# Performance work log

Measured on AMD Instinct MI355X. Metric: run time of the kernel, lower is better.

The kernel has to match this reference:

```python
import jax, jax.numpy as jnp
import numpy as np
import math

H = 8                 # num_heads
MAX_REL = 32          # max_relative_distance
VOCAB_REL = 2 * MAX_REL + 1


def setup_inputs() -> dict:
    key = jax.random.key(0)
    ks = jax.random.split(key, 8)
    B, S, D = 4, 2048, 256
    hd = D // H
    sd = 1.0 / math.sqrt(D)
    inp = {
        "query": jax.random.normal(ks[0], (B, S, D), jnp.float32),
        "mask": jnp.ones((B, 1, 1, S), jnp.float32),
        "Wq": jax.random.normal(ks[1], (D, D), jnp.float32) * sd,
        "bq": jnp.zeros((D,), jnp.float32),
        "Wk": jax.random.normal(ks[2], (D, D), jnp.float32) * sd,
        "bk": jnp.zeros((D,), jnp.float32),
        "Wv": jax.random.normal(ks[3], (D, D), jnp.float32) * sd,
        "bv": jnp.zeros((D,), jnp.float32),
        "Wo": jax.random.normal(ks[4], (D, D), jnp.float32) * sd,
        "bo": jnp.zeros((D,), jnp.float32),
        "rel_table": jax.random.normal(ks[5], (VOCAB_REL, hd), jnp.float32) * 0.1,
    }
    return inp


def _split_heads(x, B, S, hd):
    # [B,S,D] -> [B,H,S,hd]
    return x.reshape(B, S, H, hd).transpose(0, 2, 1, 3)


def _relative_row_sums(S, rel_table):
    # Original: emb = table[relpos]  (S,S,hd); scores += einsum('bhid,jkd->bhijk', Q, emb).sum(-1)
    # == einsum('bhid,jd->bhij', Q, R) with R[j,d] = sum_k emb[j,k,d].
    # Compute R without materializing the (S,S,hd) tensor: count how often each
    # relative-position bucket appears in each row, then counts @ table.
    pos = jnp.arange(S)
    relpos = jnp.clip(pos[:, None] - pos[None, :], -MAX_REL, MAX_REL) + MAX_REL  # [S,S] ints
    rows = jnp.broadcast_to(pos[:, None], (S, S))
    counts = jnp.zeros((S, VOCAB_REL), rel_table.dtype).at[
        rows.reshape(-1), relpos.reshape(-1)
    ].add(1.0)
    return counts @ rel_table  # [S, hd]


def reference(query, mask, Wq, bq, Wk, bk, Wv, bv, Wo, bo, rel_table):
    B, S, D = query.shape
    hd = D // H
    scale = 1.0 / math.sqrt(hd)

    Q = _split_heads(query @ Wq + bq, B, S, hd)
    K = _split_heads(query @ Wk + bk, B, S, hd)   # key defaults to query
    V = _split_heads(query @ Wv + bv, B, S, hd)   # value defaults to key

    scores = jnp.einsum("bhid,bhjd->bhij", Q, K) * scale
    R = _relative_row_sums(S, rel_table)          # [S, hd]
    scores = scores + jnp.einsum("bhid,jd->bhij", Q, R)

    scores = scores + (1.0 - mask) * -1e9         # mask broadcast [B,1,1,S]
    attn = jax.nn.softmax(scores, axis=-1)        # dropout is identity (training=False)

    out = jnp.einsum("bhij,bhjd->bhid", attn, V)
    out = out.transpose(0, 2, 1, 3).reshape(B, S, D)
    return out @ Wo + bo
```

## Files before the change

kernel.cpp:

```cpp
#include <hip/hip_runtime.h>
#include <hip/hip_bf16.h>
#include <math.h>

#define NH 8
#define HD 32
#define SEQ 2048
#define DM 256
#define SCALE 0.17677669529663687f
#define INV_SCALE 5.656854249492381f
#define LOG2E 1.4426950408889634f
#define QSC (SCALE * LOG2E)
#define MNEG (-1e9f * LOG2E)

typedef float f32x4 __attribute__((ext_vector_type(4)));
typedef __bf16 bf16x8 __attribute__((ext_vector_type(8)));

#define GLOAD(g, l) __builtin_amdgcn_global_load_lds( \
    (const __attribute__((address_space(1))) void*)(g), \
    (__attribute__((address_space(3))) void*)(l), 16, 0, 0)

__global__ void k_prep(const float* __restrict__ query, const float* __restrict__ mask,
                       const float* __restrict__ Wq, const float* __restrict__ Wk,
                       const float* __restrict__ Wv, const float* __restrict__ Wo,
                       const float* __restrict__ bq, const float* __restrict__ tbl,
                       __bf16* __restrict__ Xb, __bf16* __restrict__ Wt,
                       __bf16* __restrict__ WoT, float* __restrict__ MT,
                       __bf16* __restrict__ SUFn, __bf16* __restrict__ PREn,
                       float* __restrict__ WV2T, float* __restrict__ cb,
                       int* __restrict__ MFLAG) {
  const int blk = blockIdx.x, tid = threadIdx.x;
  __shared__ float ts[64][65];
  __shared__ int okl;
  if (blk < 1024) {
    size_t i = (size_t)blk * 2048 + (size_t)tid * 8;
    float4 a = *(const float4*)(query + i);
    float4 b4 = *(const float4*)(query + i + 4);
    union { __bf16 h[8]; bf16x8 v; } o;
    o.h[0] = (__bf16)a.x;  o.h[1] = (__bf16)a.y;
    o.h[2] = (__bf16)a.z;  o.h[3] = (__bf16)a.w;
    o.h[4] = (__bf16)b4.x; o.h[5] = (__bf16)b4.y;
    o.h[6] = (__bf16)b4.z; o.h[7] = (__bf16)b4.w;
    *(bf16x8*)(Xb + i) = o.v;
  } else if (blk < 1088) {
    const int idx = blk - 1024;
    const float* W;
    __bf16* dst;
    int tile;
    if (idx < 48) {
      int which = idx >> 4;
      W = which == 0 ? Wq : (which == 1 ? Wk : Wv);
      dst = Wt + which * 65536;
      tile = idx & 15;
    } else {
      W = Wo; dst = WoT; tile = idx - 48;
    }
    const int tr = (tile >> 2) * 64, tc = (tile & 3) * 64;
#pragma unroll
    for (int p = 0; p < 4; ++p) {
      int row = p * 16 + (tid >> 4);
      int col = (tid & 15) * 4;
      float4 v = *(const float4*)(W + (size_t)(tr + row) * 256 + tc + col);
      ts[row][col] = v.x; ts[row][col + 1] = v.y;
      ts[row][col + 2] = v.z; ts[row][col + 3] = v.w;
    }
    __syncthreads();
#pragma unroll
    for (int p = 0; p < 2; ++p) {
      int n = p * 32 + (tid >> 3);
      int kb = (tid & 7) * 8;
      union { __bf16 h[8]; bf16x8 v; } o;
#pragma unroll
      for (int e = 0; e < 8; ++e) o.h[e] = (__bf16)ts[kb + e][n];
      *(bf16x8*)(dst + (size_t)(tc + n) * 256 + tr + kb) = o.v;
    }
  } else if (blk == 1088) {
    if (tid == 0) okl = 1;
    __syncthreads();
    bool ok = true;
    for (int i = tid; i < 4 * SEQ; i += 256) {
      float mv = mask[i];
      MT[i] = (1.0f - mv) * MNEG;
      ok &= (mv == 1.0f);
    }
    if (!ok) atomicAnd(&okl, 0);
    __syncthreads();
    if (tid == 0) MFLAG[0] = okl;
  } else if (blk == 1089) {
    for (int idx = tid; idx < 1024; idx += 256) {
      int j = idx >> 5, d = idx & 31;
      float s = 0.f;
      for (int u = j + 33; u <= 63; ++u) s += tbl[u * 32 + d];
      SUFn[idx] = (__bf16)(-s * INV_SCALE);
    }
    for (int idx = tid; idx < 1024; idx += 256) {
      int jj = idx >> 5, d = idx & 31;
      float s = 0.f;
      for (int u = 1; u <= jj; ++u) s += tbl[u * 32 + d];
      PREn[idx] = (__bf16)(-s * INV_SCALE);
    }
  } else if (blk < 1106) {
    int tg = (blk - 1090) * 256 + tid;
    int hv = tg >> 8, k = tg & 255;
    const float* T = tbl + ((hv & 1) ? 0 : 64 * 32);
    const float* w = Wq + (size_t)k * 256 + (hv >> 1) * 32;
    float acc = 0.f;
#pragma unroll
    for (int d = 0; d < 32; ++d) acc = fmaf(w[d], T[d], acc);
    WV2T[hv * 256 + k] = acc * LOG2E;
  } else {
    if (tid < 16) {
      const float* T = tbl + ((tid & 1) ? 0 : 64 * 32);
      float a = 0.f;
#pragma unroll
      for (int d = 0; d < 32; ++d) a = fmaf(bq[(tid >> 1) * 32 + d], T[d], a);
      cb[tid] = a * LOG2E;
    }
  }
}

__launch_bounds__(256)
__global__ void k_rel(const float* __restrict__ X, const float* __restrict__ WV2T,
                      const float* __restrict__ cb, float* __restrict__ REL) {
  __shared__ float Xs[32][260];
  __shared__ float Ws[16][260];
  const int tid = threadIdx.x;
  const size_t base = (size_t)blockIdx.x * 32 * 256;
#pragma unroll
  for (int p = 0; p < 8; ++p) {
    int idx = p * 1024 + tid * 4;
    float4 v = *(const float4*)(X + base + idx);
    *(float4*)&Xs[idx >> 8][idx & 255] = v;
  }
#pragma unroll
  for (int p = 0; p < 4; ++p) {
    int idx = p * 1024 + tid * 4;
    float4 v = *(const float4*)(WV2T + idx);
    *(float4*)&Ws[idx >> 8][idx & 255] = v;
  }
  __syncthreads();
  const int hv = tid & 15, rl = tid >> 4;
  float a0 = cb[hv], a1 = a0;
  const float* xs0 = &Xs[rl][0];
  const float* xs1 = &Xs[rl + 16][0];
  const float* wsp = &Ws[hv][0];
#pragma unroll 8
  for (int k = 0; k < 256; ++k) {
    float w = wsp[k];
    a0 = fmaf(xs0[k], w, a0);
    a1 = fmaf(xs1[k], w, a1);
  }
  const int row0 = blockIdx.x * 32 + rl;
  const int h = hv >> 1, v = hv & 1;
  const int b0i = row0 >> 11, s0 = row0 & 2047;
  REL[((size_t)(b0i * NH + h) * SEQ + s0) * 2 + v] = a0;
  const int r1 = row0 + 16;
  const int b1i = r1 >> 11, s1 = r1 & 2047;
  REL[((size_t)(b1i * NH + h) * SEQ + s1) * 2 + v] = a1;
}

template <int MODE>
__launch_bounds__(256)
__global__ void k_gemm(const __bf16* __restrict__ A, const __bf16* __restrict__ Bt,
                       const float* __restrict__ b0, const float* __restrict__ b1,
                       const float* __restrict__ b2,
                       __bf16* __restrict__ Qb, __bf16* __restrict__ Kb,
                       __bf16* __restrict__ VTout, float* __restrict__ Y) {
  constexpr int BN = (MODE == 0) ? 128 : 64;
  constexpr int NFJ = BN / 32;
  __shared__ __align__(16) __bf16 As[128 * 64];
  __shared__ __align__(16) __bf16 Bs[BN * 64];
  const int tid = threadIdx.x, lane = tid & 63, wid = tid >> 6;
  const int l16 = lane & 15, lhi = lane >> 4;
  const int wr = wid >> 1, wc = wid & 1;
  const int m0 = blockIdx.x * 128, n0 = blockIdx.y * BN;

  f32x4 acc[4][NFJ];
#pragma unroll
  for (int i = 0; i < 4; ++i)
#pragma unroll
    for (int j = 0; j < NFJ; ++j) acc[i][j] = (f32x4){0.f, 0.f, 0.f, 0.f};

  for (int k0 = 0; k0 < 256; k0 += 64) {
    __syncthreads();
#pragma unroll
    for (int cc = 0; cc < 4; ++cc) {
      int cl = tid + cc * 256;
      int row = cl >> 3, kc = cl & 7;
      int k = k0 + ((kc ^ (row & 7)) * 8);
      const __bf16* src;
      if constexpr (MODE == 0) {
        src = A + (size_t)(m0 + row) * 256 + k;
      } else {
        int r = m0 + row, bb = r >> 11, s = r & 2047, h = k >> 5, dh = k & 31;
        src = A + ((size_t)(bb * NH + h) * SEQ + s) * HD + dh;
      }
      GLOAD(src, (__bf16*)As + (size_t)cl * 8);
    }
#pragma unroll
    for (int cc = 0; cc < NFJ; ++cc) {
      int cl = tid + cc * 256;
      int row = cl >> 3, kc = cl & 7;
      int k = k0 + ((kc ^ (row & 7)) * 8);
      GLOAD(Bt + (size_t)(n0 + row) * 256 + k, (__bf16*)Bs + (size_t)cl * 8);
    }
    __syncthreads();
#pragma unroll
    for (int kk = 0; kk < 64; kk += 32) {
      bf16x8 af[4], bfr[NFJ];
#pragma unroll
      for (int fi = 0; fi < 4; ++fi) {
        int row = wr * 64 + fi * 16 + l16;
        af[fi] = *(const bf16x8*)(As + row * 64 + ((((kk >> 3) + lhi) ^ (row & 7)) * 8));
      }
#pragma unroll
      for (int fj = 0; fj < NFJ; ++fj) {
        int row = wc * (BN / 2) + fj * 16 + l16;
        bfr[fj] = *(const bf16x8*)(Bs + row * 64 + ((((kk >> 3) + lhi) ^ (row & 7)) * 8));
      }
#pragma unroll
      for (int fi = 0; fi < 4; ++fi)
#pragma unroll
        for (int fj = 0; fj < NFJ; ++fj)
          acc[fi][fj] = __builtin_amdgcn_mfma_f32_16x16x32_bf16(af[fi], bfr[fj], acc[fi][fj], 0, 0, 0);
    }
  }
#pragma unroll
  for (int fi = 0; fi < 4; ++fi) {
#pragma unroll
    for (int fj = 0; fj < NFJ; ++fj) {
      int mrow = m0 + wr * 64 + fi * 16 + lhi * 4;
      int ncol = n0 + wc * (BN / 2) + fj * 16 + l16;
      if constexpr (MODE == 0) {
        int which = ncol >> 8, nw = ncol & 255, h = nw >> 5, dh = nw & 31;
        int bb = mrow >> 11, s0 = mrow & 2047;
        if (which == 2) {
          union { __bf16 h4[4]; uint2 u; } o;
#pragma unroll
          for (int r = 0; r < 4; ++r) o.h4[r] = (__bf16)(acc[fi][fj][r] + b2[nw]);
          *(uint2*)(VTout + ((size_t)(bb * NH + h) * HD + dh) * SEQ + s0) = o.u;
        } else {
          const float* bias = which == 0 ? b0 : b1;
#pragma unroll
          for (int r = 0; r < 4; ++r) {
            float v = acc[fi][fj][r] + bias[nw];
            size_t oi = ((size_t)(bb * NH + h) * SEQ + (s0 + r)) * HD + dh;
            if (which == 0) Qb[oi] = (__bf16)(v * QSC);
            else Kb[oi] = (__bf16)v;
          }
        }
      } else {
#pragma unroll
        for (int r = 0; r < 4; ++r)
          Y[(size_t)(mrow + r) * 256 + ncol] = acc[fi][fj][r] + b0[ncol];
      }
    }
  }
}

__launch_bounds__(512, 4)
__global__ void k_flash(const __bf16* __restrict__ Qb, const __bf16* __restrict__ Kb,
                        const __bf16* __restrict__ VT, const float* __restrict__ REL,
                        const __bf16* __restrict__ SUFn, const __bf16* __restrict__ PREn,
                        const float* __restrict__ MT, const int* __restrict__ MFLAG,
                        __bf16* __restrict__ Ob) {
  const int bh = blockIdx.y, qt = blockIdx.x, b = bh >> 3;
  const int tid = threadIdx.x, wid = tid >> 6, lane = tid & 63;
  const int l16 = lane & 15, lhi = lane >> 4;

  __shared__ __align__(16) __bf16 kbuf[2][128 * 32];
  __shared__ __align__(16) __bf16 vbuf[2][32 * 128];
  __shared__ __align__(16) __bf16 plds[8][16 * 128];

  const int qrow = qt * 128 + wid * 16 + l16;
  const size_t rg = (size_t)bh * SEQ + qrow;
  const bf16x8 qfrag = *(const bf16x8*)(Qb + rg * HD + lhi * 8);
  const float2 uw = *(const float2*)(REL + rg * 2);
  const float uu = uw.x, ww = uw.y, duw = uu - ww;
  const float duw16 = 16.f * duw;
  const f32x4 duwr = {0.f, duw, 2.f * duw, 3.f * duw};
  const int flag = MFLAG[0];

  const int kj = tid >> 2, kc = tid & 3;
  const __bf16* ksrc = Kb + (size_t)bh * SEQ * HD + (size_t)kj * HD + ((kc ^ ((kj >> 1) & 3)) * 8);
  const int vd = tid >> 4, vc = tid & 15;
  const __bf16* vsrc = VT + ((size_t)bh * HD + vd) * SEQ + ((vc ^ (vd & 7)) * 8);

  f32x4 of0 = {0.f, 0.f, 0.f, 0.f}, of1 = {0.f, 0.f, 0.f, 0.f}, of2 = {0.f, 0.f, 0.f, 0.f};
  const f32x4 zero4 = {0.f, 0.f, 0.f, 0.f}; (void)zero4;
  bf16x8 ones;
#pragma unroll
  for (int e = 0; e < 8; ++e) ones[e] = (__bf16)1.0f;
  float m = -3.0e38f;
  __bf16* pl = &plds[wid][0];
  const float* mtp = MT + b * SEQ + lhi * 4;

  GLOAD(ksrc, &kbuf[0][(size_t)tid * 8]);
  GLOAD(vsrc, &vbuf[0][(size_t)tid * 8]);
  __syncthreads();

  for (int t = 0, cur = 0; t < 16; ++t, cur ^= 1) {
    const int jb = t * 128;
    if (t < 15) {
      GLOAD(ksrc + (size_t)(jb + 128) * HD, &kbuf[cur ^ 1][(size_t)tid * 8]);
      GLOAD(vsrc + (jb + 128), &vbuf[cur ^ 1][(size_t)tid * 8]);
    }
    const __bf16* kb = kbuf[cur];
    const __bf16* vb = vbuf[cur];

    f32x4 lin = duwr + (float)(jb + lhi * 4) * duw;
    f32x4 sf[8];
    __builtin_amdgcn_s_setprio(1);
#pragma unroll
    for (int jt = 0; jt < 8; ++jt) {
      const int row = jt * 16 + l16;
      bf16x8 kf = *(const bf16x8*)(kb + row * 32 + ((lhi ^ ((row >> 1) & 3)) * 8));
      sf[jt] = __builtin_amdgcn_mfma_f32_16x16x32_bf16(kf, qfrag, lin, 0, 0, 0);
      lin += duw16;
    }
    __builtin_amdgcn_s_setprio(0);

    if (t == 0) {
      const bf16x8 s0 = *(const bf16x8*)(SUFn + l16 * HD + lhi * 8);
      const bf16x8 s1 = *(const bf16x8*)(SUFn + (16 + l16) * HD + lhi * 8);
      sf[0] = __builtin_amdgcn_mfma_f32_16x16x32_bf16(s0, qfrag, sf[0], 0, 0, 0);
      sf[1] = __builtin_amdgcn_mfma_f32_16x16x32_bf16(s1, qfrag, sf[1], 0, 0, 0);
#pragma unroll
      for (int jt = 0; jt < 2; ++jt)
#pragma unroll
        for (int r = 0; r < 4; ++r)
          sf[jt][r] += fmaxf(31.f - (float)(jt * 16 + lhi * 4 + r), 0.f) * uu;
    }
    if (t == 15) {
      const bf16x8 p0 = *(const bf16x8*)(PREn + l16 * HD + lhi * 8);
      const bf16x8 p1 = *(const bf16x8*)(PREn + (16 + l16) * HD + lhi * 8);
      sf[6] = __builtin_amdgcn_mfma_f32_16x16x32_bf16(p0, qfrag, sf[6], 0, 0, 0);
      sf[7] = __builtin_amdgcn_mfma_f32_16x16x32_bf16(p1, qfrag, sf[7], 0, 0, 0);
#pragma unroll
      for (int jt = 6; jt < 8; ++jt)
#pragma unroll
        for (int r = 0; r < 4; ++r)
          sf[jt][r] += fmaxf((float)(1920 + jt * 16 + lhi * 4 + r) - 2016.f, 0.f) * ww;
    }
    if (!flag) {
#pragma unroll
      for (int jt = 0; jt < 8; ++jt)
        sf[jt] += *(const f32x4*)(mtp + jb + jt * 16);
    }

    float tmax = -3.0e38f;
#pragma unroll
    for (int jt = 0; jt < 8; ++jt)
      tmax = fmaxf(tmax, fmaxf(fmaxf(sf[jt].x, sf[jt].y), fmaxf(sf[jt].z, sf[jt].w)));
    tmax = fmaxf(tmax, __shfl_xor(tmax, 16));
    tmax = fmaxf(tmax, __shfl_xor(tmax, 32));
    const float mn = fmaxf(m, tmax);
    const float c = __builtin_amdgcn_exp2f(m - mn);
    m = mn;
    of0 *= c; of1 *= c; of2 *= c;

#pragma unroll
    for (int jt = 0; jt < 8; ++jt) {
      union { __bf16 h4[4]; uint2 u; } pk;
#pragma unroll
      for (int r = 0; r < 4; ++r)
        pk.h4[r] = (__bf16)__builtin_amdgcn_exp2f(sf[jt][r] - m);
      const int blk16 = ((jt * 2 + (lhi >> 1)) ^ (l16 & 7));
      *(uint2*)(pl + l16 * 128 + blk16 * 8 + (lhi & 1) * 4) = pk.u;
    }

    __builtin_amdgcn_s_setprio(1);
#pragma unroll
    for (int kt = 0; kt < 4; ++kt) {
      const int pblk = (kt * 4 + lhi) ^ (l16 & 7);
      bf16x8 pf = *(const bf16x8*)(pl + l16 * 128 + pblk * 8);
      bf16x8 v0 = *(const bf16x8*)(vb + l16 * 128 + (((kt * 4 + lhi) ^ (l16 & 7)) * 8));
      bf16x8 v1 = *(const bf16x8*)(vb + (16 + l16) * 128 + (((kt * 4 + lhi) ^ (l16 & 7)) * 8));
      of0 = __builtin_amdgcn_mfma_f32_16x16x32_bf16(v0, pf, of0, 0, 0, 0);
      of1 = __builtin_amdgcn_mfma_f32_16x16x32_bf16(v1, pf, of1, 0, 0, 0);
      of2 = __builtin_amdgcn_mfma_f32_16x16x32_bf16(ones, pf, of2, 0, 0, 0);
    }
    __builtin_amdgcn_s_setprio(0);
    __syncthreads();
  }

  const float inv = 1.0f / of2[0];
  union { __bf16 h4[4]; uint2 u; } o0, o1;
#pragma unroll
  for (int r = 0; r < 4; ++r) {
    o0.h4[r] = (__bf16)(of0[r] * inv);
    o1.h4[r] = (__bf16)(of1[r] * inv);
  }
  *(uint2*)(Ob + rg * HD + lhi * 4) = o0.u;
  *(uint2*)(Ob + rg * HD + 16 + lhi * 4) = o1.u;
}

extern "C" void kernel_launch(void* const* d_in, const int* in_sizes, int n_in,
                              void* d_out, int out_size, void* d_ws, size_t ws_size,
                              hipStream_t stream) {
  (void)in_sizes; (void)n_in; (void)out_size; (void)ws_size;
  const float* query = (const float*)d_in[0];
  const float* mask  = (const float*)d_in[1];
  const float* Wq = (const float*)d_in[2];
  const float* bq = (const float*)d_in[3];
  const float* Wk = (const float*)d_in[4];
  const float* bk = (const float*)d_in[5];
  const float* Wv = (const float*)d_in[6];
  const float* bv = (const float*)d_in[7];
  const float* Wo = (const float*)d_in[8];
  const float* bo = (const float*)d_in[9];
  const float* tbl = (const float*)d_in[10];
  float* out = (float*)d_out;
  char* ws = (char*)d_ws;

  const size_t MB = 1024ull * 1024;
  __bf16* Xb    = (__bf16*)(ws);
  __bf16* Wt    = (__bf16*)(ws + 4 * MB);
  __bf16* WoT   = (__bf16*)(ws + 4 * MB + 393216);
  __bf16* SUFn  = (__bf16*)(ws + 4 * MB + 524288);
  __bf16* PREn  = (__bf16*)(ws + 4 * MB + 526336);
  float*  WV2T  = (float*) (ws + 4 * MB + 528384);
  float*  cbv   = (float*) (ws + 4 * MB + 544768);
  float*  MT    = (float*) (ws + 4 * MB + 544832);
  int*    MFLAG = (int*)   (ws + 4 * MB + 577600);
  float*  REL   = (float*) (ws + 5 * MB);
  __bf16* Qb    = (__bf16*)(ws + 6 * MB);
  __bf16* Kb    = (__bf16*)(ws + 10 * MB);
  __bf16* VT    = (__bf16*)(ws + 14 * MB);
  __bf16* Ob    = (__bf16*)(ws + 18 * MB);

  k_prep<<<1107, 256, 0, stream>>>(query, mask, Wq, Wk, Wv, Wo, bq, tbl,
                                   Xb, Wt, WoT, MT, SUFn, PREn, WV2T, cbv, MFLAG);
  k_rel<<<256, 256, 0, stream>>>(query, WV2T, cbv, REL);
  k_gemm<0><<<dim3(64, 6), 256, 0, stream>>>(Xb, Wt, bq, bk, bv, Qb, Kb, VT, nullptr);
  k_flash<<<dim3(16, 32), 512, 0, stream>>>(Qb, Kb, VT, REL, SUFn, PREn, MT, MFLAG, Ob);
  k_gemm<1><<<dim3(64, 4), 256, 0, stream>>>(Ob, WoT, bo, nullptr, nullptr,
                                             nullptr, nullptr, nullptr, out);
}
```

Baseline: 89.65 us.

## Split P staging into two halves, hoist linear bias, remap flash block order

The flash kernel now precomputes the per-column linear relative-bias term once, as constant accumulator seeds. The per-tile offset jb*duw is folded into the running max instead of being added to every score. The softmax-exp, P store and PV MFMA stage is split into two half-tile phases, which halves the P LDS buffer and lets the exp work of one half interleave with the MFMAs of the other. The grid is flattened to 1D with a block-to-(batch,head) mapping that spreads heads across XCDs for cache locality. The max is computed on unshifted scores, which slightly changes numerical rounding, and it adds 32 registers for c0.

```diff
diff --git a/kernel.cpp b/kernel.cpp
--- a/kernel.cpp
+++ b/kernel.cpp
@@ -263,30 +263,39 @@
                         const __bf16* __restrict__ SUFn, const __bf16* __restrict__ PREn,
                         const float* __restrict__ MT, const int* __restrict__ MFLAG,
                         __bf16* __restrict__ Ob) {
-  const int bh = blockIdx.y, qt = blockIdx.x, b = bh >> 3;
+  const int bid = blockIdx.x;
+  const int bh = (bid & 7) * 4 + ((bid >> 3) & 3);
+  const int qt = bid >> 5;
+  const int b = bh >> 3;
   const int tid = threadIdx.x, wid = tid >> 6, lane = tid & 63;
   const int l16 = lane & 15, lhi = lane >> 4;
 
   __shared__ __align__(16) __bf16 kbuf[2][128 * 32];
   __shared__ __align__(16) __bf16 vbuf[2][32 * 128];
-  __shared__ __align__(16) __bf16 plds[8][16 * 128];
+  __shared__ __align__(16) __bf16 plds[8][16 * 64];
 
   const int qrow = qt * 128 + wid * 16 + l16;
   const size_t rg = (size_t)bh * SEQ + qrow;
   const bf16x8 qfrag = *(const bf16x8*)(Qb + rg * HD + lhi * 8);
   const float2 uw = *(const float2*)(REL + rg * 2);
   const float uu = uw.x, ww = uw.y, duw = uu - ww;
-  const float duw16 = 16.f * duw;
-  const f32x4 duwr = {0.f, duw, 2.f * duw, 3.f * duw};
   const int flag = MFLAG[0];
 
+  f32x4 c0[8];
+  {
+    const f32x4 cr = {(float)(lhi * 4) * duw, (float)(lhi * 4 + 1) * duw,
+                      (float)(lhi * 4 + 2) * duw, (float)(lhi * 4 + 3) * duw};
+#pragma unroll
+    for (int jt = 0; jt < 8; ++jt)
+      c0[jt] = cr + (float)(jt * 16) * duw;
+  }
+
   const int kj = tid >> 2, kc = tid & 3;
-  const __bf16* ksrc = Kb + (size_t)bh * SEQ * HD + (size_t)kj * HD + ((kc ^ ((kj >> 1) & 3)) * 8);
+  const __bf16* ksrc = Kb + ((size_t)bh * SEQ + kj) * HD + ((kc ^ ((kj >> 1) & 3)) * 8);
   const int vd = tid >> 4, vc = tid & 15;
   const __bf16* vsrc = VT + ((size_t)bh * HD + vd) * SEQ + ((vc ^ (vd & 7)) * 8);
 
   f32x4 of0 = {0.f, 0.f, 0.f, 0.f}, of1 = {0.f, 0.f, 0.f, 0.f}, of2 = {0.f, 0.f, 0.f, 0.f};
-  const f32x4 zero4 = {0.f, 0.f, 0.f, 0.f}; (void)zero4;
   bf16x8 ones;
 #pragma unroll
   for (int e = 0; e < 8; ++e) ones[e] = (__bf16)1.0f;
@@ -307,15 +316,13 @@
     const __bf16* kb = kbuf[cur];
     const __bf16* vb = vbuf[cur];
 
-    f32x4 lin = duwr + (float)(jb + lhi * 4) * duw;
     f32x4 sf[8];
     __builtin_amdgcn_s_setprio(1);
 #pragma unroll
     for (int jt = 0; jt < 8; ++jt) {
       const int row = jt * 16 + l16;
       bf16x8 kf = *(const bf16x8*)(kb + row * 32 + ((lhi ^ ((row >> 1) & 3)) * 8));
-      sf[jt] = __builtin_amdgcn_mfma_f32_16x16x32_bf16(kf, qfrag, lin, 0, 0, 0);
-      lin += duw16;
+      sf[jt] = __builtin_amdgcn_mfma_f32_16x16x32_bf16(kf, qfrag, c0[jt], 0, 0, 0);
     }
     __builtin_amdgcn_s_setprio(0);
 
@@ -339,7 +346,7 @@
       for (int jt = 6; jt < 8; ++jt)
 #pragma unroll
         for (int r = 0; r < 4; ++r)
-          sf[jt][r] += fmaxf((float)(1920 + jt * 16 + lhi * 4 + r) - 2016.f, 0.f) * ww;
+          sf[jt][r] += fmaxf((float)(jb + jt * 16 + lhi * 4 + r) - 2016.f, 0.f) * ww;
     }
     if (!flag) {
 #pragma unroll
@@ -347,39 +354,43 @@
         sf[jt] += *(const f32x4*)(mtp + jb + jt * 16);
     }
 
+    const float tsp = (float)jb * duw;
     float tmax = -3.0e38f;
 #pragma unroll
     for (int jt = 0; jt < 8; ++jt)
-      tmax = fmaxf(tmax, fmaxf(fmaxf(sf[jt].x, sf[jt].y), fmaxf(sf[jt].z, sf[jt].w)));
+      tmax = fmaxf(fmaxf(fmaxf(fmaxf(tmax, sf[jt].x), sf[jt].y), sf[jt].z), sf[jt].w);
     tmax = fmaxf(tmax, __shfl_xor(tmax, 16));
     tmax = fmaxf(tmax, __shfl_xor(tmax, 32));
-    const float mn = fmaxf(m, tmax);
+    const float mn = fmaxf(m, tmax + tsp);
     const float c = __builtin_amdgcn_exp2f(m - mn);
     m = mn;
+    const float m2 = mn - tsp;
     of0 *= c; of1 *= c; of2 *= c;
 
 #pragma unroll
-    for (int jt = 0; jt < 8; ++jt) {
-      union { __bf16 h4[4]; uint2 u; } pk;
-#pragma unroll
-      for (int r = 0; r < 4; ++r)
-        pk.h4[r] = (__bf16)__builtin_amdgcn_exp2f(sf[jt][r] - m);
-      const int blk16 = ((jt * 2 + (lhi >> 1)) ^ (l16 & 7));
-      *(uint2*)(pl + l16 * 128 + blk16 * 8 + (lhi & 1) * 4) = pk.u;
-    }
-
-    __builtin_amdgcn_s_setprio(1);
-#pragma unroll
-    for (int kt = 0; kt < 4; ++kt) {
-      const int pblk = (kt * 4 + lhi) ^ (l16 & 7);
-      bf16x8 pf = *(const bf16x8*)(pl + l16 * 128 + pblk * 8);
-      bf16x8 v0 = *(const bf16x8*)(vb + l16 * 128 + (((kt * 4 + lhi) ^ (l16 & 7)) * 8));
-      bf16x8 v1 = *(const bf16x8*)(vb + (16 + l16) * 128 + (((kt * 4 + lhi) ^ (l16 & 7)) * 8));
-      of0 = __builtin_amdgcn_mfma_f32_16x16x32_bf16(v0, pf, of0, 0, 0, 0);
-      of1 = __builtin_amdgcn_mfma_f32_16x16x32_bf16(v1, pf, of1, 0, 0, 0);
-      of2 = __builtin_amdgcn_mfma_f32_16x16x32_bf16(ones, pf, of2, 0, 0, 0);
-    }
-    __builtin_amdgcn_s_setprio(0);
+    for (int ph = 0; ph < 2; ++ph) {
+#pragma unroll
+      for (int jt = ph * 4; jt < ph * 4 + 4; ++jt) {
+        union { __bf16 h4[4]; uint2 u; } pk;
+#pragma unroll
+        for (int r = 0; r < 4; ++r)
+          pk.h4[r] = (__bf16)__builtin_amdgcn_exp2f(sf[jt][r] - m2);
+        const int blk16 = (((jt & 3) * 2 + (lhi >> 1)) ^ (l16 & 7));
+        *(uint2*)(pl + l16 * 64 + blk16 * 8 + (lhi & 1) * 4) = pk.u;
+      }
+      __builtin_amdgcn_s_setprio(1);
+#pragma unroll
+      for (int kt = ph * 2; kt < ph * 2 + 2; ++kt) {
+        const int pblk = (((kt & 1) * 4 + lhi) ^ (l16 & 7));
+        bf16x8 pf = *(const bf16x8*)(pl + l16 * 64 + pblk * 8);
+        bf16x8 v0 = *(const bf16x8*)(vb + l16 * 128 + (((kt * 4 + lhi) ^ (l16 & 7)) * 8));
+        bf16x8 v1 = *(const bf16x8*)(vb + (16 + l16) * 128 + (((kt * 4 + lhi) ^ (l16 & 7)) * 8));
+        of0 = __builtin_amdgcn_mfma_f32_16x16x32_bf16(v0, pf, of0, 0, 0, 0);
+        of1 = __builtin_amdgcn_mfma_f32_16x16x32_bf16(v1, pf, of1, 0, 0, 0);
+        of2 = __builtin_amdgcn_mfma_f32_16x16x32_bf16(ones, pf, of2, 0, 0, 0);
+      }
+      __builtin_amdgcn_s_setprio(0);
+    }
     __syncthreads();
   }
 
@@ -432,7 +443,7 @@
                                    Xb, Wt, WoT, MT, SUFn, PREn, WV2T, cbv, MFLAG);
   k_rel<<<256, 256, 0, stream>>>(query, WV2T, cbv, REL);
   k_gemm<0><<<dim3(64, 6), 256, 0, stream>>>(Xb, Wt, bq, bk, bv, Qb, Kb, VT, nullptr);
-  k_flash<<<dim3(16, 32), 512, 0, stream>>>(Qb, Kb, VT, REL, SUFn, PREn, MT, MFLAG, Ob);
+  k_flash<<<512, 512, 0, stream>>>(Qb, Kb, VT, REL, SUFn, PREn, MT, MFLAG, Ob);
   k_gemm<1><<<dim3(64, 4), 256, 0, stream>>>(Ob, WoT, bo, nullptr, nullptr,
                                              nullptr, nullptr, nullptr, out);
 }
```

Measured after the change: 91.14 us, median of 2. About the same (+1.7%).
